# Kernel optimization log

Hardware: AMD Instinct MI355X
Metric: run time of the kernel (lower is better)

Reference implementation:

```python
import jax, jax.numpy as jnp
import numpy as np

N = 2048          # num_nodes
A = 100           # anchor count (hard-coded in _select_anchor_points)


def setup_inputs() -> dict:
    key = jax.random.key(0)
    k1, k2, k3 = jax.random.split(key, 3)
    motifGraph = jax.random.uniform(k1, (N, N), dtype=jnp.float32)
    node_weights = jax.random.uniform(k2, (N,), dtype=jnp.float32)
    weight_matrix = jax.random.uniform(k3, (N, A), dtype=jnp.float32)
    sigma = jnp.array(1.0, dtype=jnp.float32)
    return {"motifGraph": motifGraph, "node_weights": node_weights,
            "weight_matrix": weight_matrix, "sigma": sigma}


def _floyd_warshall(w):
    # w: [n,n] edge-weight matrix (inf = no edge, 0 on diagonal)
    n = w.shape[0]
    def step(d, k):
        # d_ij = min(d_ij, d_ik + d_kj)
        d = jnp.minimum(d, d[:, k][:, None] + d[k, :][None, :])
        return d, None
    d, _ = jax.lax.scan(step, w, jnp.arange(n))
    return d


def reference(motifGraph, node_weights, weight_matrix, sigma):
    n = motifGraph.shape[0]
    # _adjust_motif_graph: row-scale by node weights. The original detaches
    # before the scipy floyd_warshall call, so no grad flows through it.
    adj = jax.lax.stop_gradient(motifGraph * node_weights[:n, None])
    # csr_matrix semantics: zero entries are "no edge"; directed=False takes
    # the min of w_ij and w_ji; diagonal distance is 0.
    w = jnp.where(adj > 0, adj, jnp.inf)
    w = jnp.minimum(w, w.T)
    idx = jnp.arange(n)
    w = w.at[idx, idx].set(0.0)
    dist = _floyd_warshall(w)
    dist = jnp.where(jnp.isinf(dist), 100.0, dist)
    # _select_anchor_points: top-100 node weights (all indices < n here)
    anchors = jnp.argsort(-jax.lax.stop_gradient(node_weights))[:A]
    consensus_vectors = dist[:, anchors]                      # [n, A]
    distance_sums = (consensus_vectors.sum(axis=1) - 100.0).sum() / (n * A)
    weighted = weight_matrix[:n, :] * consensus_vectors       # [n, A]
    # build_consensus_graph: cdist(...)**4 == (squared euclidean dist)**2
    xx = jnp.sum(weighted * weighted, axis=1)                 # [n]
    sq = jnp.maximum(xx[:, None] + xx[None, :] - 2.0 * weighted @ weighted.T, 0.0)
    consensus_graph = jnp.exp(-(sq * sq) / (2.0 * sigma ** 2))
    return consensus_vectors, distance_sums, consensus_graph
```

## Files before the change

### kernel.cpp

```cpp
#include <hip/hip_runtime.h>
#include <hip/hip_cooperative_groups.h>
#include <stdint.h>

namespace cg = cooperative_groups;

#define NN 2048
#define AA 100
#define NT 32

template<bool AL> __device__ __forceinline__ float4 ld4(const float* __restrict__ p) {
  if (AL) return *(const float4*)p;
  return make_float4(p[0], p[1], p[2], p[3]);
}
template<bool AL> __device__ __forceinline__ void st4(float* __restrict__ p, float4 v) {
  if (AL) { *(float4*)p = v; }
  else { p[0] = v.x; p[1] = v.y; p[2] = v.z; p[3] = v.w; }
}

__device__ __forceinline__ void minplus16(const float (*A)[68], const float (*B)[68],
                                          float c[4][4], int i0, int j0) {
#pragma unroll 4
  for (int k4 = 0; k4 < 16; ++k4) {
    const int k = k4 * 4;
    float4 a0 = *(const float4*)&A[i0 + 0][k];
    float4 a1 = *(const float4*)&A[i0 + 1][k];
    float4 a2 = *(const float4*)&A[i0 + 2][k];
    float4 a3 = *(const float4*)&A[i0 + 3][k];
    float4 b0 = *(const float4*)&B[k + 0][j0];
    float4 b1 = *(const float4*)&B[k + 1][j0];
    float4 b2 = *(const float4*)&B[k + 2][j0];
    float4 b3 = *(const float4*)&B[k + 3][j0];
#define MP1(ii, jj, f)                                                           \
    c[ii][jj] = fminf(fminf(fminf(fminf(c[ii][jj], a##ii.x + b0.f),              \
                                  a##ii.y + b1.f),                               \
                            a##ii.z + b2.f),                                     \
                      a##ii.w + b3.f)
#define MP_ROW(ii) MP1(ii, 0, x); MP1(ii, 1, y); MP1(ii, 2, z); MP1(ii, 3, w)
    MP_ROW(0); MP_ROW(1); MP_ROW(2); MP_ROW(3);
#undef MP_ROW
#undef MP1
  }
}

__device__ __forceinline__ void close_seq(float (*S)[68], float c[4][4],
                                          int i0, int j0, int ty, int tx) {
  for (int kb = 0; kb < 16; ++kb) {
#pragma unroll
    for (int kq = 0; kq < 4; ++kq) {
      const int k = kb * 4 + kq;
      float4 br = *(const float4*)&S[k][j0];
      float a0 = S[i0 + 0][k];
      float a1 = S[i0 + 1][k];
      float a2 = S[i0 + 2][k];
      float a3 = S[i0 + 3][k];
      c[0][0] = fminf(c[0][0], a0 + br.x); c[0][1] = fminf(c[0][1], a0 + br.y);
      c[0][2] = fminf(c[0][2], a0 + br.z); c[0][3] = fminf(c[0][3], a0 + br.w);
      c[1][0] = fminf(c[1][0], a1 + br.x); c[1][1] = fminf(c[1][1], a1 + br.y);
      c[1][2] = fminf(c[1][2], a1 + br.z); c[1][3] = fminf(c[1][3], a1 + br.w);
      c[2][0] = fminf(c[2][0], a2 + br.x); c[2][1] = fminf(c[2][1], a2 + br.y);
      c[2][2] = fminf(c[2][2], a2 + br.z); c[2][3] = fminf(c[2][3], a2 + br.w);
      c[3][0] = fminf(c[3][0], a3 + br.x); c[3][1] = fminf(c[3][1], a3 + br.y);
      c[3][2] = fminf(c[3][2], a3 + br.z); c[3][3] = fminf(c[3][3], a3 + br.w);
      const int kn = k + 1;
      const int ii = (kq + 1) & 3;
      if (kn < 64) {
        if ((kn >> 2) == ty)
          *(float4*)&S[kn][j0] = make_float4(c[ii][0], c[ii][1], c[ii][2], c[ii][3]);
        if ((kn >> 2) == tx) {
          S[i0 + 0][kn] = c[0][ii];
          S[i0 + 1][kn] = c[1][ii];
          S[i0 + 2][kn] = c[2][ii];
          S[i0 + 3][kn] = c[3][ii];
        }
      }
      __syncthreads();
    }
  }
}

__global__ __launch_bounds__(256, 4) void fw_persist(
    const float* __restrict__ mg, const float* __restrict__ nw,
    float* __restrict__ dist) {
  __shared__ __align__(16) float As[64][68];
  __shared__ __align__(16) float Bs[64][68];
  const int bx = blockIdx.x, by = blockIdx.y;
  const int t = threadIdx.x;
  const int tx = t & 15, ty = t >> 4;
  const int i0 = ty * 4, j0 = tx * 4;
  cg::grid_group grid = cg::this_grid();

#pragma unroll
  for (int l = 0; l < 4; ++l) {
    int idx = l * 256 + t;
    int r = idx >> 4, c4 = (idx & 15) * 4;
    float4 g = *(const float4*)&mg[(bx * 64 + r) * NN + by * 64 + c4];
    Bs[c4 + 0][r] = g.x; Bs[c4 + 1][r] = g.y;
    Bs[c4 + 2][r] = g.z; Bs[c4 + 3][r] = g.w;
  }
  __syncthreads();
  float c[4][4];
  {
    float4 nwj = *(const float4*)&nw[bx * 64 + j0];
#pragma unroll
    for (int ii = 0; ii < 4; ++ii) {
      int rl = i0 + ii;
      int i = by * 64 + rl;
      float nwi = nw[i];
      float4 m = *(const float4*)&mg[i * NN + bx * 64 + j0];
      float4 bt = *(const float4*)&Bs[rl][j0];
      float av[4] = {m.x * nwi, m.y * nwi, m.z * nwi, m.w * nwi};
      float bv[4] = {bt.x * nwj.x, bt.y * nwj.y, bt.z * nwj.z, bt.w * nwj.w};
#pragma unroll
      for (int q = 0; q < 4; ++q) {
        float wa = av[q] > 0.0f ? av[q] : __builtin_huge_valf();
        float wb = bv[q] > 0.0f ? bv[q] : __builtin_huge_valf();
        float v = fminf(wa, wb);
        if (i == bx * 64 + j0 + q) v = 0.0f;
        c[ii][q] = v;
      }
    }
  }
  if (bx == 0 && by == 0) {
#pragma unroll
    for (int ii = 0; ii < 4; ++ii)
      *(float4*)&As[i0 + ii][j0] = make_float4(c[ii][0], c[ii][1], c[ii][2], c[ii][3]);
    __syncthreads();
    close_seq(As, c, i0, j0, ty, tx);
#pragma unroll
    for (int ii = 0; ii < 4; ++ii)
      *(float4*)&dist[(i0 + ii) * NN + j0] =
          make_float4(c[ii][0], c[ii][1], c[ii][2], c[ii][3]);
    __threadfence();
  }
  grid.sync();
  __threadfence();

  for (int r = 0; r < NT; ++r) {
    const bool isDiag = (by == r) && (bx == r);
    const bool isRow  = (by == r) && !isDiag;
    const bool isCol  = (bx == r) && !isDiag;
    if (isRow || isCol) {
      float (*Da)[68] = isRow ? As : Bs;
      float (*Ow)[68] = isRow ? Bs : As;
      const float* db = &dist[(r * 64) * NN + r * 64];
#pragma unroll
      for (int l = 0; l < 4; ++l) {
        int idx = l * 256 + t;
        int row = idx >> 4, c4 = (idx & 15) * 4;
        *(float4*)&Da[row][c4] = *(const float4*)&db[row * NN + c4];
      }
#pragma unroll
      for (int ii = 0; ii < 4; ++ii)
        *(float4*)&Ow[i0 + ii][j0] = make_float4(c[ii][0], c[ii][1], c[ii][2], c[ii][3]);
      __syncthreads();
      minplus16(As, Bs, c, i0, j0);
      float* ob = &dist[(by * 64) * NN + bx * 64];
#pragma unroll
      for (int ii = 0; ii < 4; ++ii)
        *(float4*)&ob[(i0 + ii) * NN + j0] =
            make_float4(c[ii][0], c[ii][1], c[ii][2], c[ii][3]);
      __threadfence();
    }
    grid.sync();
    __threadfence();
    if (by != r && bx != r) {
      const bool closer = (bx == r + 1) && (by == r + 1) && (r + 1 < NT);
      if (closer) __builtin_amdgcn_s_setprio(1);
      const float* ab = &dist[(by * 64) * NN + r * 64];
      const float* bb = &dist[(r * 64) * NN + bx * 64];
#pragma unroll
      for (int l = 0; l < 4; ++l) {
        int idx = l * 256 + t;
        int row = idx >> 4, c4 = (idx & 15) * 4;
        *(float4*)&As[row][c4] = *(const float4*)&ab[row * NN + c4];
        *(float4*)&Bs[row][c4] = *(const float4*)&bb[row * NN + c4];
      }
      __syncthreads();
      minplus16(As, Bs, c, i0, j0);
      if (closer) {
        __syncthreads();
#pragma unroll
        for (int ii = 0; ii < 4; ++ii)
          *(float4*)&As[i0 + ii][j0] = make_float4(c[ii][0], c[ii][1], c[ii][2], c[ii][3]);
        __syncthreads();
        close_seq(As, c, i0, j0, ty, tx);
        float* ob = &dist[((r + 1) * 64) * NN + (r + 1) * 64];
#pragma unroll
        for (int ii = 0; ii < 4; ++ii)
          *(float4*)&ob[(i0 + ii) * NN + j0] =
              make_float4(c[ii][0], c[ii][1], c[ii][2], c[ii][3]);
        __builtin_amdgcn_s_setprio(0);
        __threadfence();
      }
    }
    grid.sync();
    __threadfence();
  }

  float* ob = &dist[(by * 64) * NN + bx * 64];
#pragma unroll
  for (int ii = 0; ii < 4; ++ii)
    *(float4*)&ob[(i0 + ii) * NN + j0] =
        make_float4(c[ii][0], c[ii][1], c[ii][2], c[ii][3]);
}

template<bool AL>
__global__ __launch_bounds__(256) void build_w_kernel(
    const float* __restrict__ mg, const float* __restrict__ nw,
    float* __restrict__ w) {
  __shared__ float Tt[64][65];
  __shared__ __align__(16) float As[64][68];
  int bi = blockIdx.y, bj = blockIdx.x;
  int t = threadIdx.x;
  const bool diag0 = (bi == 0) && (bj == 0);
#pragma unroll
  for (int l = 0; l < 4; ++l) {
    int idx = l * 256 + t;
    int r = idx >> 4, c4 = (idx & 15) * 4;
    float4 g = *(const float4*)&mg[(bj * 64 + r) * NN + bi * 64 + c4];
    Tt[c4 + 0][r] = g.x; Tt[c4 + 1][r] = g.y;
    Tt[c4 + 2][r] = g.z; Tt[c4 + 3][r] = g.w;
  }
  __syncthreads();
#pragma unroll
  for (int l = 0; l < 4; ++l) {
    int idx = l * 256 + t;
    int r = idx >> 4, c4 = (idx & 15) * 4;
    int i = bi * 64 + r, j = bj * 64 + c4;
    float4 m = *(const float4*)&mg[i * NN + j];
    float4 nwj = *(const float4*)&nw[j];
    float nwi = nw[i];
    float av[4] = {m.x * nwi, m.y * nwi, m.z * nwi, m.w * nwi};
    float bv[4] = {Tt[r][c4 + 0] * nwj.x, Tt[r][c4 + 1] * nwj.y,
                   Tt[r][c4 + 2] * nwj.z, Tt[r][c4 + 3] * nwj.w};
    float vv[4];
#pragma unroll
    for (int q = 0; q < 4; ++q) {
      float wa = av[q] > 0.0f ? av[q] : __builtin_huge_valf();
      float wb = bv[q] > 0.0f ? bv[q] : __builtin_huge_valf();
      float v = fminf(wa, wb);
      if (i == j + q) v = 0.0f;
      vv[q] = v;
    }
    float4 v4 = make_float4(vv[0], vv[1], vv[2], vv[3]);
    if (diag0) {
      *(float4*)&As[r][c4] = v4;
    } else {
      st4<AL>(&w[i * NN + j], v4);
    }
  }
  if (diag0) {
    __syncthreads();
    int tx = t & 15, ty = t >> 4;
    int i0 = ty * 4, j0 = tx * 4;
    float c[4][4];
#pragma unroll
    for (int ii = 0; ii < 4; ++ii) {
      float4 q = *(const float4*)&As[i0 + ii][j0];
      c[ii][0] = q.x; c[ii][1] = q.y; c[ii][2] = q.z; c[ii][3] = q.w;
    }
    close_seq(As, c, i0, j0, ty, tx);
#pragma unroll
    for (int ii = 0; ii < 4; ++ii)
      st4<AL>(&w[(i0 + ii) * NN + j0],
              make_float4(c[ii][0], c[ii][1], c[ii][2], c[ii][3]));
  }
}

template<bool AL>
__global__ __launch_bounds__(256) void fw_p2(float* __restrict__ d, int r) {
  __shared__ __align__(16) float As[64][68];
  __shared__ __align__(16) float Bs[64][68];
  int tile = blockIdx.x, side = blockIdx.y;
  if (tile == r) return;
  int t = threadIdx.x;
  int dbase = (r * 64) * NN + r * 64;
  int obase = (side == 0) ? (r * 64) * NN + tile * 64
                          : (tile * 64) * NN + r * 64;
  float (*Da)[68] = (side == 0) ? As : Bs;
  float (*Ow)[68] = (side == 0) ? Bs : As;
#pragma unroll
  for (int l = 0; l < 4; ++l) {
    int idx = l * 256 + t;
    int row = idx >> 4, c4 = (idx & 15) * 4;
    *(float4*)&Da[row][c4] = ld4<AL>(&d[dbase + row * NN + c4]);
    *(float4*)&Ow[row][c4] = ld4<AL>(&d[obase + row * NN + c4]);
  }
  int tx = t & 15, ty = t >> 4;
  int i0 = ty * 4, j0 = tx * 4;
  __syncthreads();
  float c[4][4];
#pragma unroll
  for (int ii = 0; ii < 4; ++ii) {
    float4 q = *(const float4*)&Ow[i0 + ii][j0];
    c[ii][0] = q.x; c[ii][1] = q.y; c[ii][2] = q.z; c[ii][3] = q.w;
  }
  minplus16(As, Bs, c, i0, j0);
#pragma unroll
  for (int ii = 0; ii < 4; ++ii)
    st4<AL>(&d[obase + (i0 + ii) * NN + j0],
            make_float4(c[ii][0], c[ii][1], c[ii][2], c[ii][3]));
}

template<bool AL>
__global__ __launch_bounds__(256) void fw_p3(float* __restrict__ d, int r) {
  __shared__ __align__(16) float As[64][68];
  __shared__ __align__(16) float Bs[64][68];
  int bx = blockIdx.x, by = blockIdx.y;
  if (bx == r || by == r) return;
  int t = threadIdx.x;
#pragma unroll
  for (int l = 0; l < 4; ++l) {
    int idx = l * 256 + t;
    int row = idx >> 4, c4 = (idx & 15) * 4;
    *(float4*)&As[row][c4] = ld4<AL>(&d[(by * 64 + row) * NN + r * 64 + c4]);
    *(float4*)&Bs[row][c4] = ld4<AL>(&d[(r * 64 + row) * NN + bx * 64 + c4]);
  }
  int tx = t & 15, ty = t >> 4;
  int i0 = ty * 4, j0 = tx * 4;
  int obase = (by * 64) * NN + bx * 64;
  float c[4][4];
#pragma unroll
  for (int ii = 0; ii < 4; ++ii) {
    float4 q = ld4<AL>(&d[obase + (i0 + ii) * NN + j0]);
    c[ii][0] = q.x; c[ii][1] = q.y; c[ii][2] = q.z; c[ii][3] = q.w;
  }
  __syncthreads();
  minplus16(As, Bs, c, i0, j0);

  bool closer = (bx == r + 1) && (by == r + 1) && (r + 1 < NT);
  if (closer) {
    __syncthreads();
#pragma unroll
    for (int ii = 0; ii < 4; ++ii)
      *(float4*)&As[i0 + ii][j0] = make_float4(c[ii][0], c[ii][1], c[ii][2], c[ii][3]);
    __syncthreads();
    close_seq(As, c, i0, j0, ty, tx);
  }
#pragma unroll
  for (int ii = 0; ii < 4; ++ii)
    st4<AL>(&d[obase + (i0 + ii) * NN + j0],
            make_float4(c[ii][0], c[ii][1], c[ii][2], c[ii][3]));
}

__global__ __launch_bounds__(256) void anchors_kernel(
    const float* __restrict__ nw, int* __restrict__ anchors) {
  __shared__ __align__(16) float s[NN];
  int t = threadIdx.x;
#pragma unroll
  for (int l = 0; l < NN / 256; ++l) s[l * 256 + t] = nw[l * 256 + t];
  __syncthreads();
  int i = blockIdx.x * 64 + (t >> 2);
  int q = t & 3;
  float wi = s[i];
  int rank = 0;
  int jb = q * (NN / 4);
  for (int j = jb; j < jb + NN / 4; j += 4) {
    float4 v = *(const float4*)&s[j];
    rank += (int)(v.x > wi) + ((int)(v.x == wi) & (int)(j + 0 < i));
    rank += (int)(v.y > wi) + ((int)(v.y == wi) & (int)(j + 1 < i));
    rank += (int)(v.z > wi) + ((int)(v.z == wi) & (int)(j + 2 < i));
    rank += (int)(v.w > wi) + ((int)(v.w == wi) & (int)(j + 3 < i));
  }
  rank += __shfl_xor(rank, 1);
  rank += __shfl_xor(rank, 2);
  if (q == 0 && rank < AA) anchors[rank] = i;
}

__global__ __launch_bounds__(256) void cv_kernel(
    const float* __restrict__ dist, const int* __restrict__ anchors,
    float* __restrict__ cv_out, float* __restrict__ sum_acc) {
  int idx = blockIdx.x * 256 + threadIdx.x;
  int i = idx / 100, a = idx - i * 100;
  float dv = dist[i * NN + anchors[a]];
  if (isinf(dv)) dv = 100.0f;
  cv_out[idx] = dv;
  float v = dv;
#pragma unroll
  for (int off = 32; off > 0; off >>= 1) v += __shfl_down(v, off);
  __shared__ float sv[4];
  int lane = threadIdx.x & 63, w = threadIdx.x >> 6;
  if (lane == 0) sv[w] = v;
  __syncthreads();
  if (threadIdx.x == 0) atomicAdd(sum_acc, sv[0] + sv[1] + sv[2] + sv[3]);
}

__global__ __launch_bounds__(256) void graph_kernel(
    const float* __restrict__ wm, const float* __restrict__ cv,
    const float* __restrict__ sigma, float* __restrict__ graph) {
  __shared__ __align__(16) float As[64][108];
  __shared__ __align__(16) float Bs[64][108];
  __shared__ float xs[64], ys[64];
  int bx = blockIdx.x, by = blockIdx.y;
  int t = threadIdx.x;
#pragma unroll
  for (int l = 0; l < 7; ++l) {
    int idx = l * 256 + t;
    if (idx < 1600) {
      int row = idx / 25, c4 = (idx - row * 25) * 4;
      float4 wa = *(const float4*)&wm[(by * 64 + row) * AA + c4];
      float4 ca = *(const float4*)&cv[(by * 64 + row) * AA + c4];
      *(float4*)&As[row][c4] =
          make_float4(wa.x * ca.x, wa.y * ca.y, wa.z * ca.z, wa.w * ca.w);
      float4 wb = *(const float4*)&wm[(bx * 64 + row) * AA + c4];
      float4 cb = *(const float4*)&cv[(bx * 64 + row) * AA + c4];
      *(float4*)&Bs[row][c4] =
          make_float4(wb.x * cb.x, wb.y * cb.y, wb.z * cb.z, wb.w * cb.w);
    }
  }
  __syncthreads();
  if (t < 64) {
    float s = 0.0f;
    for (int k4 = 0; k4 < 25; ++k4) {
      float4 q = *(const float4*)&As[t][k4 * 4];
      s += q.x * q.x + q.y * q.y + q.z * q.z + q.w * q.w;
    }
    xs[t] = s;
  } else if (t < 128) {
    int r = t - 64;
    float s = 0.0f;
    for (int k4 = 0; k4 < 25; ++k4) {
      float4 q = *(const float4*)&Bs[r][k4 * 4];
      s += q.x * q.x + q.y * q.y + q.z * q.z + q.w * q.w;
    }
    ys[r] = s;
  }
  __syncthreads();
  int tx = t & 15, ty = t >> 4;
  float acc[4][4] = {{0.0f}};
#pragma unroll 5
  for (int k4 = 0; k4 < 25; ++k4) {
    int k = k4 * 4;
    float4 a_[4], b_[4];
#pragma unroll
    for (int ii = 0; ii < 4; ++ii) a_[ii] = *(const float4*)&As[ty + 16 * ii][k];
#pragma unroll
    for (int jj = 0; jj < 4; ++jj) b_[jj] = *(const float4*)&Bs[tx + 16 * jj][k];
#pragma unroll
    for (int ii = 0; ii < 4; ++ii)
#pragma unroll
      for (int jj = 0; jj < 4; ++jj)
        acc[ii][jj] += a_[ii].x * b_[jj].x + a_[ii].y * b_[jj].y +
                       a_[ii].z * b_[jj].z + a_[ii].w * b_[jj].w;
  }
  float s = *sigma;
  float inv2s2 = 0.5f / (s * s);
#pragma unroll
  for (int ii = 0; ii < 4; ++ii) {
    int gi = by * 64 + ty + 16 * ii;
    float xi = xs[ty + 16 * ii];
#pragma unroll
    for (int jj = 0; jj < 4; ++jj) {
      int gj = bx * 64 + tx + 16 * jj;
      float sq = fmaxf(xi + ys[tx + 16 * jj] - 2.0f * acc[ii][jj], 0.0f);
      graph[gi * NN + gj] = __expf(-(sq * sq) * inv2s2);
    }
  }
}

__global__ void finalize_kernel(const float* __restrict__ sum_acc,
                                float* __restrict__ out) {
  if (threadIdx.x == 0)
    *out = (*sum_acc - 204800.0f) / 204800.0f;
}

template<bool AL>
static void run_fw_fallback(const float* mg, const float* nw, float* dist,
                            hipStream_t stream) {
  build_w_kernel<AL><<<dim3(NT, NT), 256, 0, stream>>>(mg, nw, dist);
  for (int r = 0; r < NT; ++r) {
    fw_p2<AL><<<dim3(NT, 2), 256, 0, stream>>>(dist, r);
    fw_p3<AL><<<dim3(NT, NT), 256, 0, stream>>>(dist, r);
  }
}

static bool coop_ok() {
  static int ok = -1;
  if (ok < 0) {
    int dev = 0;
    (void)hipGetDevice(&dev);
    int coopAttr = 0;
    (void)hipDeviceGetAttribute(&coopAttr, hipDeviceAttributeCooperativeLaunch, dev);
    int cus = 0;
    (void)hipDeviceGetAttribute(&cus, hipDeviceAttributeMultiprocessorCount, dev);
    int nb = 0;
    hipError_t e = hipOccupancyMaxActiveBlocksPerMultiprocessor(&nb, fw_persist, 256, 0);
    ok = (e == hipSuccess && coopAttr && nb > 0 && (long)nb * cus >= NT * NT) ? 1 : 0;
  }
  return ok == 1;
}

extern "C" void kernel_launch(void* const* d_in, const int* in_sizes, int n_in,
                              void* d_out, int out_size, void* d_ws, size_t ws_size,
                              hipStream_t stream) {
  (void)in_sizes; (void)n_in; (void)out_size;
  const float* mg    = (const float*)d_in[0];
  const float* nw    = (const float*)d_in[1];
  const float* wm    = (const float*)d_in[2];
  const float* sigma = (const float*)d_in[3];
  float* out        = (float*)d_out;
  float* cv_out     = out;
  float* scalar_out = out + 204800;
  float* graph_out  = out + 204801;

  float* W = (float*)d_ws;
  float* sum_acc = W;
  int* anchors   = (int*)(W + 4);
  const bool bigws = ws_size >= (size_t)(256 + (size_t)NN * NN) * sizeof(float);
  float* dist = bigws ? (W + 256) : graph_out;
  const bool al = ((((uintptr_t)dist) & 15) == 0);

  hipMemsetAsync(sum_acc, 0, sizeof(float), stream);

  bool launched = false;
  if (bigws && al && coop_ok()) {
    void* args[] = {(void*)&mg, (void*)&nw, (void*)&dist};
    hipError_t ce = hipLaunchCooperativeKernel(fw_persist, dim3(NT, NT),
                                               dim3(256, 1, 1), args, 0, stream);
    launched = (ce == hipSuccess);
  }
  if (!launched) {
    if (al) run_fw_fallback<true>(mg, nw, dist, stream);
    else    run_fw_fallback<false>(mg, nw, dist, stream);
  }

  anchors_kernel<<<NN / 64, 256, 0, stream>>>(nw, anchors);
  cv_kernel<<<800, 256, 0, stream>>>(dist, anchors, cv_out, sum_acc);
  graph_kernel<<<dim3(NT, NT), 256, 0, stream>>>(wm, cv_out, sigma, graph_out);
  finalize_kernel<<<1, 64, 0, stream>>>(sum_acc, scalar_out);
}
```

Measured before the change: 1.080 ms.

## Replace grid-wide barriers with per-tile dataflow flags in persistent Floyd-Warshall

Removes the two grid.sync barriers per round in the cooperative blocked Floyd-Warshall kernel. Blocks now wait on per-tile ready flags in global memory that are set after the diagonal, row and column tiles are computed. Those tiles are published to separate contiguous 64x64 staging buffers rather than strided dist writes. This lets independent tiles proceed as soon as their dependencies are ready instead of waiting on the slowest block each phase. The cost is spin-waiting with sleep, extra workspace and memset of the flag area, and correctness that depends on the memory ordering of relaxed loads plus fences.

```diff
diff --git a/kernel.cpp b/kernel.cpp
--- a/kernel.cpp
+++ b/kernel.cpp
@@ -1,12 +1,13 @@
 #include <hip/hip_runtime.h>
-#include <hip/hip_cooperative_groups.h>
 #include <stdint.h>
-
-namespace cg = cooperative_groups;
 
 #define NN 2048
 #define AA 100
 #define NT 32
+
+#define F_DIAG 256
+#define F_ROW  512
+#define F_COL  1536
 
 template<bool AL> __device__ __forceinline__ float4 ld4(const float* __restrict__ p) {
   if (AL) return *(const float4*)p;
@@ -78,16 +79,48 @@
   }
 }
 
+template<int LAZY>
+__device__ __forceinline__ void waitflag(int* f) {
+  int it = 0;
+  while (__hip_atomic_load(f, __ATOMIC_RELAXED, __HIP_MEMORY_SCOPE_AGENT) == 0) {
+    if (++it > 24) __builtin_amdgcn_s_sleep(LAZY);
+  }
+}
+__device__ __forceinline__ void setflag(int* f) {
+  __hip_atomic_store(f, 1, __ATOMIC_RELEASE, __HIP_MEMORY_SCOPE_AGENT);
+}
+
+__device__ __forceinline__ void stage64(const float* __restrict__ g,
+                                        float (*S)[68], int t) {
+#pragma unroll
+  for (int l = 0; l < 4; ++l) {
+    int idx = l * 256 + t;
+    int row = idx >> 4, c4 = (idx & 15) * 4;
+    *(float4*)&S[row][c4] = *(const float4*)&g[row * 64 + c4];
+  }
+}
+__device__ __forceinline__ void pub64(float* __restrict__ g,
+                                      const float c[4][4], int i0, int j0) {
+#pragma unroll
+  for (int ii = 0; ii < 4; ++ii)
+    *(float4*)&g[(i0 + ii) * 64 + j0] =
+        make_float4(c[ii][0], c[ii][1], c[ii][2], c[ii][3]);
+}
+
 __global__ __launch_bounds__(256, 4) void fw_persist(
     const float* __restrict__ mg, const float* __restrict__ nw,
-    float* __restrict__ dist) {
+    float* __restrict__ dist, int* __restrict__ Wi,
+    float* __restrict__ diagb, float* __restrict__ rowb,
+    float* __restrict__ colb) {
   __shared__ __align__(16) float As[64][68];
   __shared__ __align__(16) float Bs[64][68];
   const int bx = blockIdx.x, by = blockIdx.y;
   const int t = threadIdx.x;
   const int tx = t & 15, ty = t >> 4;
   const int i0 = ty * 4, j0 = tx * 4;
-  cg::grid_group grid = cg::this_grid();
+  int* DIAGF = Wi + F_DIAG;
+  int* ROWF  = Wi + F_ROW;
+  int* COLF  = Wi + F_COL;
 
 #pragma unroll
   for (int l = 0; l < 4; ++l) {
@@ -121,80 +154,72 @@
     }
   }
   if (bx == 0 && by == 0) {
+    __syncthreads();
 #pragma unroll
     for (int ii = 0; ii < 4; ++ii)
       *(float4*)&As[i0 + ii][j0] = make_float4(c[ii][0], c[ii][1], c[ii][2], c[ii][3]);
     __syncthreads();
     close_seq(As, c, i0, j0, ty, tx);
-#pragma unroll
-    for (int ii = 0; ii < 4; ++ii)
-      *(float4*)&dist[(i0 + ii) * NN + j0] =
-          make_float4(c[ii][0], c[ii][1], c[ii][2], c[ii][3]);
-    __threadfence();
-  }
-  grid.sync();
-  __threadfence();
+    pub64(diagb, c, i0, j0);
+    __syncthreads();
+    if (t == 0) { __threadfence(); setflag(DIAGF + 0); }
+  }
 
   for (int r = 0; r < NT; ++r) {
-    const bool isDiag = (by == r) && (bx == r);
-    const bool isRow  = (by == r) && !isDiag;
-    const bool isCol  = (bx == r) && !isDiag;
-    if (isRow || isCol) {
-      float (*Da)[68] = isRow ? As : Bs;
+    if (by == r && bx == r) continue;
+    if (by == r || bx == r) {
+      const bool isRow = (by == r);
+      __syncthreads();
       float (*Ow)[68] = isRow ? Bs : As;
-      const float* db = &dist[(r * 64) * NN + r * 64];
-#pragma unroll
-      for (int l = 0; l < 4; ++l) {
-        int idx = l * 256 + t;
-        int row = idx >> 4, c4 = (idx & 15) * 4;
-        *(float4*)&Da[row][c4] = *(const float4*)&db[row * NN + c4];
+#pragma unroll
+      for (int ii = 0; ii < 4; ++ii)
+        *(float4*)&Ow[i0 + ii][j0] =
+            make_float4(c[ii][0], c[ii][1], c[ii][2], c[ii][3]);
+      if (t == 0) { waitflag<1>(DIAGF + r); __threadfence(); }
+      __syncthreads();
+      stage64(diagb + r * 4096, isRow ? As : Bs, t);
+      __syncthreads();
+      minplus16(As, Bs, c, i0, j0);
+      float* ob = isRow ? rowb + (r * NT + bx) * 4096
+                        : colb + (by * NT + r) * 4096;
+      pub64(ob, c, i0, j0);
+      __syncthreads();
+      if (t == 0) {
+        __threadfence();
+        setflag(isRow ? ROWF + r * NT + bx : COLF + by * NT + r);
       }
-#pragma unroll
-      for (int ii = 0; ii < 4; ++ii)
-        *(float4*)&Ow[i0 + ii][j0] = make_float4(c[ii][0], c[ii][1], c[ii][2], c[ii][3]);
-      __syncthreads();
-      minplus16(As, Bs, c, i0, j0);
-      float* ob = &dist[(by * 64) * NN + bx * 64];
-#pragma unroll
-      for (int ii = 0; ii < 4; ++ii)
-        *(float4*)&ob[(i0 + ii) * NN + j0] =
-            make_float4(c[ii][0], c[ii][1], c[ii][2], c[ii][3]);
-      __threadfence();
-    }
-    grid.sync();
-    __threadfence();
-    if (by != r && bx != r) {
+    } else {
       const bool closer = (bx == r + 1) && (by == r + 1) && (r + 1 < NT);
       if (closer) __builtin_amdgcn_s_setprio(1);
-      const float* ab = &dist[(by * 64) * NN + r * 64];
-      const float* bb = &dist[(r * 64) * NN + bx * 64];
-#pragma unroll
-      for (int l = 0; l < 4; ++l) {
-        int idx = l * 256 + t;
-        int row = idx >> 4, c4 = (idx & 15) * 4;
-        *(float4*)&As[row][c4] = *(const float4*)&ab[row * NN + c4];
-        *(float4*)&Bs[row][c4] = *(const float4*)&bb[row * NN + c4];
+      if (t == 0) {
+        if (closer) {
+          waitflag<1>(ROWF + r * NT + bx);
+          waitflag<1>(COLF + by * NT + r);
+        } else {
+          waitflag<8>(ROWF + r * NT + bx);
+          waitflag<8>(COLF + by * NT + r);
+        }
+        __threadfence();
       }
+      __syncthreads();
+      stage64(colb + (by * NT + r) * 4096, As, t);
+      stage64(rowb + (r * NT + bx) * 4096, Bs, t);
       __syncthreads();
       minplus16(As, Bs, c, i0, j0);
       if (closer) {
         __syncthreads();
 #pragma unroll
         for (int ii = 0; ii < 4; ++ii)
-          *(float4*)&As[i0 + ii][j0] = make_float4(c[ii][0], c[ii][1], c[ii][2], c[ii][3]);
+          *(float4*)&As[i0 + ii][j0] =
+              make_float4(c[ii][0], c[ii][1], c[ii][2], c[ii][3]);
         __syncthreads();
         close_seq(As, c, i0, j0, ty, tx);
-        float* ob = &dist[((r + 1) * 64) * NN + (r + 1) * 64];
-#pragma unroll
-        for (int ii = 0; ii < 4; ++ii)
-          *(float4*)&ob[(i0 + ii) * NN + j0] =
-              make_float4(c[ii][0], c[ii][1], c[ii][2], c[ii][3]);
+        pub64(diagb + (r + 1) * 4096, c, i0, j0);
+        __syncthreads();
+        if (t == 0) { __threadfence(); setflag(DIAGF + r + 1); }
         __builtin_amdgcn_s_setprio(0);
-        __threadfence();
       }
     }
-    grid.sync();
-    __threadfence();
   }
 
   float* ob = &dist[(by * 64) * NN + bx * 64];
@@ -506,15 +531,23 @@
   float* W = (float*)d_ws;
   float* sum_acc = W;
   int* anchors   = (int*)(W + 4);
-  const bool bigws = ws_size >= (size_t)(256 + (size_t)NN * NN) * sizeof(float);
-  float* dist = bigws ? (W + 256) : graph_out;
+  const size_t needP = (size_t)(16384 + (size_t)NN * NN + NT * 4096 +
+                                2 * (size_t)NT * NT * 4096) * sizeof(float);
+  const bool bigP  = ws_size >= needP;
+  const bool bigF  = ws_size >= (size_t)(2048 + (size_t)NN * NN) * sizeof(float);
+  float* dist = bigP ? (W + 16384) : (bigF ? (W + 2048) : graph_out);
   const bool al = ((((uintptr_t)dist) & 15) == 0);
 
-  hipMemsetAsync(sum_acc, 0, sizeof(float), stream);
+  (void)hipMemsetAsync(W, 0, 16384, stream);
 
   bool launched = false;
-  if (bigws && al && coop_ok()) {
-    void* args[] = {(void*)&mg, (void*)&nw, (void*)&dist};
+  if (bigP && al && coop_ok()) {
+    int* Wi = (int*)W;
+    float* diagb = dist + (size_t)NN * NN;
+    float* rowb  = diagb + NT * 4096;
+    float* colb  = rowb + (size_t)NT * NT * 4096;
+    void* args[] = {(void*)&mg, (void*)&nw, (void*)&dist, (void*)&Wi,
+                    (void*)&diagb, (void*)&rowb, (void*)&colb};
     hipError_t ce = hipLaunchCooperativeKernel(fw_persist, dim3(NT, NT),
                                                dim3(256, 1, 1), args, 0, stream);
     launched = (ce == hipSuccess);
```

Measured after the change: 1.084 ms. Within noise of the previous version (+0.4%).
